# Kernel optimization log

Hardware: AMD Instinct MI355X
Metric: run time of the kernel (lower is better)

Reference implementation:

```python
import jax, jax.numpy as jnp
import numpy as np

R = 8          # shuffle_rate
HEADS = 4
DIM_HEAD = 64


def setup_inputs() -> dict:
    key = jax.random.key(0)
    k1, k2, k3 = jax.random.split(key, 3)
    dim = 64
    C = dim * R * R            # 4096, token channel dim after unshuffle
    inner = HEADS * DIM_HEAD   # 256
    x = jax.random.normal(k1, (8, dim, 256, 256), dtype=jnp.float32)
    W_qkv = jax.random.normal(k2, (C, 3 * inner), dtype=jnp.float32) * (C ** -0.5)
    W_out = jax.random.normal(k3, (inner, C), dtype=jnp.float32) * (inner ** -0.5)
    b_out = jnp.zeros((C,), dtype=jnp.float32)
    return {"x": x, "W_qkv": W_qkv, "W_out": W_out, "b_out": b_out}


def reference(x, W_qkv, W_out, b_out):
    scale = DIM_HEAD ** -0.5
    B, C0, H0, W0 = x.shape
    h, w = H0 // R, W0 // R
    N = h * w
    C = C0 * R * R
    # PixelUnshuffle: [B,C0,H0,W0] -> [B, C0*R*R, h, w]
    xd = x.reshape(B, C0, h, R, w, R).transpose(0, 1, 3, 5, 2, 4).reshape(B, C, h, w)
    # flatten spatial -> tokens [B, N, C]
    tokens = xd.reshape(B, C, N).transpose(0, 2, 1)
    qkv = tokens @ W_qkv                                   # [B, N, 3*inner]
    q, k, v = jnp.split(qkv, 3, axis=-1)
    def heads(t):  # [B,N,inner] -> [B,H,N,d]
        return t.reshape(B, N, HEADS, DIM_HEAD).transpose(0, 2, 1, 3)
    q, k, v = heads(q), heads(k), heads(v)
    dots = jnp.einsum('bhnd,bhmd->bhnm', q, k) * scale
    attn = jax.nn.softmax(dots, axis=-1)
    out = jnp.einsum('bhnm,bhmd->bhnd', attn, v)
    out = out.transpose(0, 2, 1, 3).reshape(B, N, HEADS * DIM_HEAD)
    y = out @ W_out + b_out                                # [B, N, C]
    y = y.transpose(0, 2, 1).reshape(B, C, h, w)
    # PixelShuffle: [B, C0*R*R, h, w] -> [B, C0, H0, W0]
    y = y.reshape(B, C0, R, R, h, w).transpose(0, 1, 4, 2, 5, 3).reshape(B, C0, H0, W0)
    return y
```

## Files before the change

### kernel.cpp

```cpp
#include <hip/hip_runtime.h>

typedef unsigned short u16;
typedef __attribute__((ext_vector_type(8))) short s16x8;
typedef __attribute__((ext_vector_type(4))) short s16x4;
typedef __attribute__((ext_vector_type(4))) float f32x4;

__device__ __forceinline__ u16 f2bf(float f) {
    unsigned int u;
    __builtin_memcpy(&u, &f, 4);
    unsigned int r = u + 0x7FFFu + ((u >> 16) & 1u);
    return (u16)(r >> 16);
}

__device__ __forceinline__ void gl_lds16(const u16* g, u16* l) {
    __builtin_amdgcn_global_load_lds(
        (const __attribute__((address_space(1))) unsigned int*)g,
        (__attribute__((address_space(3))) unsigned int*)l,
        16, 0, 0);
}

__global__ __launch_bounds__(256) void k_unshuffle(const float* __restrict__ x,
                                                   u16* __restrict__ tok) {
    int idx = blockIdx.x * 256 + threadIdx.x;
    int r1  = idx & 7;
    int xxg = (idx >> 3) & 7;
    int yy  = (idx >> 6) & 31;
    int c0  = (idx >> 11) & 63;
    int b   = idx >> 17;

    const float* src = x + ((size_t)((b * 64 + c0) * 256 + yy * 8 + r1)) * 256 + xxg * 32;
    int mbase = b * 1024 + yy * 32 + xxg * 4;
    int cbase = c0 * 64 + r1 * 8;
    for (int q = 0; q < 4; ++q) {
        float4 f0 = *(const float4*)(src + q * 8);
        float4 f1 = *(const float4*)(src + q * 8 + 4);
        s16x8 v;
        v[0] = (short)f2bf(f0.x); v[1] = (short)f2bf(f0.y);
        v[2] = (short)f2bf(f0.z); v[3] = (short)f2bf(f0.w);
        v[4] = (short)f2bf(f1.x); v[5] = (short)f2bf(f1.y);
        v[6] = (short)f2bf(f1.z); v[7] = (short)f2bf(f1.w);
        *(s16x8*)(tok + (size_t)(mbase + q) * 4096 + cbase) = v;
    }
}

__global__ __launch_bounds__(256) void k_transpose(const float* __restrict__ in,
                                                   u16* __restrict__ out,
                                                   int rows, int cols) {
    __shared__ float tile[64][65];
    int bx = blockIdx.x * 64, by = blockIdx.y * 64;
    int tx = threadIdx.x & 63, ty = threadIdx.x >> 6;
    for (int i = ty; i < 64; i += 4)
        tile[i][tx] = in[(size_t)(by + i) * cols + bx + tx];
    __syncthreads();
    for (int i = ty; i < 64; i += 4)
        out[(size_t)(bx + i) * rows + by + tx] = f2bf(tile[tx][i]);
}

__global__ __launch_bounds__(256) void k_gemm_qkv(const u16* __restrict__ A,
                                                  const u16* __restrict__ Bt,
                                                  float* __restrict__ P) {
    const int K = 4096;
    __shared__ u16 As[128 * 64];
    __shared__ u16 Bs[128 * 64];
    const int tid = threadIdx.x;
    const int wave = tid >> 6, lane = tid & 63;
    const int quad = lane >> 4, l15 = lane & 15;
    const int wm = wave >> 1, wn = wave & 1;
    const int tm = blockIdx.y * 128, tn = blockIdx.x * 128;
    const int z = blockIdx.z;

    f32x4 acc[4][4] = {};

    for (int k0 = z * 2048; k0 < (z + 1) * 2048; k0 += 64) {
        __syncthreads();
        for (int t = 0; t < 4; ++t) {
            int c = wave * 256 + t * 64 + lane;
            int row = c >> 3, kc = c & 7;
            gl_lds16(A + (size_t)(tm + row) * K + k0 + kc * 8,
                     As + (wave * 256 + t * 64) * 8);
        }
        for (int t = 0; t < 4; ++t) {
            int c = wave * 256 + t * 64 + lane;
            int row = c >> 3, kc = c & 7;
            gl_lds16(Bt + (size_t)(tn + row) * K + k0 + kc * 8,
                     Bs + (wave * 256 + t * 64) * 8);
        }
        __syncthreads();
        for (int kk = 0; kk < 64; kk += 32) {
            s16x8 af[4], bf[4];
            for (int i = 0; i < 4; ++i)
                af[i] = *(const s16x8*)(As + (wm * 64 + i * 16 + l15) * 64 + kk + quad * 8);
            for (int j = 0; j < 4; ++j)
                bf[j] = *(const s16x8*)(Bs + (wn * 64 + j * 16 + l15) * 64 + kk + quad * 8);
            for (int i = 0; i < 4; ++i)
                for (int j = 0; j < 4; ++j)
                    acc[i][j] = __builtin_amdgcn_mfma_f32_16x16x32_bf16(af[i], bf[j], acc[i][j], 0, 0, 0);
        }
    }

    float* Pz = P + (size_t)z * 8192 * 768;
    for (int i = 0; i < 4; ++i) {
        int mb = tm + wm * 64 + i * 16 + quad * 4;
        for (int j = 0; j < 4; ++j) {
            int col = tn + wn * 64 + j * 16 + l15;
            for (int r = 0; r < 4; ++r)
                Pz[(size_t)(mb + r) * 768 + col] = acc[i][j][r];
        }
    }
}

__global__ __launch_bounds__(256) void k_qkv_reduce(const float* __restrict__ P,
                                                    u16* __restrict__ Qo,
                                                    u16* __restrict__ Ko,
                                                    u16* __restrict__ Vt) {
    __shared__ u16 tile[64][65];
    const int tid = threadIdx.x;
    const int ct = blockIdx.x, mt = blockIdx.y;
    const int c_l = tid & 63;
    const int col = ct * 64 + c_l;
    const int mbase = mt * 64;
    const float* P1 = P + (size_t)8192 * 768;

    if (ct < 8) {
        int which = col >> 8;
        int h = (col >> 6) & 3, d = col & 63;
        u16* dst = (which == 0) ? Qo : Ko;
        for (int k = 0; k < 16; ++k) {
            int m = mbase + (tid >> 6) + k * 4;
            float v = P[(size_t)m * 768 + col] + P1[(size_t)m * 768 + col];
            int b = m >> 10, n = m & 1023;
            dst[((size_t)((b * 4 + h) * 1024 + n)) * 64 + d] = f2bf(v);
        }
    } else {
        int h = ct - 8;
        int b = mbase >> 10;
        int nbase = mbase & 1023;
        for (int k = 0; k < 16; ++k) {
            int ml = (tid >> 6) + k * 4;
            int m = mbase + ml;
            float v = P[(size_t)m * 768 + col] + P1[(size_t)m * 768 + col];
            tile[ml][c_l] = f2bf(v);
        }
        __syncthreads();
        for (int k = 0; k < 16; ++k) {
            int d = (tid >> 6) + k * 4;
            Vt[((size_t)((b * 4 + h) * 64 + d)) * 1024 + nbase + c_l] = tile[c_l][d];
        }
    }
}

__global__ __launch_bounds__(256) void k_attn(const u16* __restrict__ Qb,
                                              const u16* __restrict__ Kb,
                                              const u16* __restrict__ Vt,
                                              u16* __restrict__ aout) {
    const int bh = blockIdx.y;
    const int q0 = blockIdx.x * 64;
    const int tid = threadIdx.x;
    const int wave = tid >> 6, lane = tid & 63;
    const int quad = lane >> 4, l15 = lane & 15;
    const size_t base = (size_t)bh * 1024 * 64;
    const float scale = 0.125f;

    __shared__ u16 Ks[64 * 64];
    __shared__ u16 Vts[64 * 68];
    __shared__ u16 Ps[4][16 * 64];

    s16x8 aq0, aq1;
    {
        const u16* qp = Qb + base + (size_t)(q0 + wave * 16 + l15) * 64 + quad * 8;
        aq0 = *(const s16x8*)(qp);
        aq1 = *(const s16x8*)(qp + 32);
    }

    float m_i[4], l_i[4];
    f32x4 o[4] = {};
    for (int r = 0; r < 4; ++r) { m_i[r] = -1e30f; l_i[r] = 0.f; }

    const int vrow = tid >> 2, vpart = tid & 3;

    for (int t = 0; t < 16; ++t) {
        __syncthreads();
        for (int e = 0; e < 2; ++e) {
            int s = e * 256 + tid;
            gl_lds16(Kb + base + (size_t)t * 4096 + s * 8, Ks + s * 8);
        }
        {
            const u16* src = Vt + base + (size_t)vrow * 1024 + t * 64 + vpart * 16;
            s16x8 a = *(const s16x8*)(src);
            s16x8 b2 = *(const s16x8*)(src + 8);
            *(s16x8*)(Vts + vrow * 68 + vpart * 16) = a;
            *(s16x8*)(Vts + vrow * 68 + vpart * 16 + 8) = b2;
        }
        __syncthreads();

        f32x4 s4[4];
        for (int j = 0; j < 4; ++j) {
            const u16* kr = Ks + (j * 16 + l15) * 64 + quad * 8;
            s16x8 b0 = *(const s16x8*)(kr);
            s16x8 b1 = *(const s16x8*)(kr + 32);
            f32x4 c = {};
            c = __builtin_amdgcn_mfma_f32_16x16x32_bf16(aq0, b0, c, 0, 0, 0);
            c = __builtin_amdgcn_mfma_f32_16x16x32_bf16(aq1, b1, c, 0, 0, 0);
            s4[j] = c;
        }

        for (int r = 0; r < 4; ++r) {
            float sv0 = s4[0][r] * scale, sv1 = s4[1][r] * scale;
            float sv2 = s4[2][r] * scale, sv3 = s4[3][r] * scale;
            float mt = fmaxf(fmaxf(sv0, sv1), fmaxf(sv2, sv3));
            for (int off = 1; off < 16; off <<= 1)
                mt = fmaxf(mt, __shfl_xor(mt, off, 64));
            float mn = fmaxf(m_i[r], mt);
            float alpha = __expf(m_i[r] - mn);
            m_i[r] = mn;
            float p0 = __expf(sv0 - mn), p1 = __expf(sv1 - mn);
            float p2 = __expf(sv2 - mn), p3 = __expf(sv3 - mn);
            u16* pw = Ps[wave] + (quad * 4 + r) * 64 + l15;
            pw[0]  = f2bf(p0);
            pw[16] = f2bf(p1);
            pw[32] = f2bf(p2);
            pw[48] = f2bf(p3);
            float rs = p0 + p1 + p2 + p3;
            for (int off = 1; off < 16; off <<= 1)
                rs += __shfl_xor(rs, off, 64);
            l_i[r] = l_i[r] * alpha + rs;
            for (int dt = 0; dt < 4; ++dt) o[dt][r] *= alpha;
        }

        for (int kk = 0; kk < 64; kk += 32) {
            s16x8 pf = *(const s16x8*)(Ps[wave] + l15 * 64 + kk + quad * 8);
            for (int dt = 0; dt < 4; ++dt) {
                const u16* vr = Vts + (dt * 16 + l15) * 68 + kk + quad * 8;
                s16x4 v0 = *(const s16x4*)(vr);
                s16x4 v1 = *(const s16x4*)(vr + 4);
                s16x8 vf;
                vf[0] = v0[0]; vf[1] = v0[1]; vf[2] = v0[2]; vf[3] = v0[3];
                vf[4] = v1[0]; vf[5] = v1[1]; vf[6] = v1[2]; vf[7] = v1[3];
                o[dt] = __builtin_amdgcn_mfma_f32_16x16x32_bf16(pf, vf, o[dt], 0, 0, 0);
            }
        }
    }

    int b = bh >> 2, h = bh & 3;
    float rl[4];
    for (int r = 0; r < 4; ++r) rl[r] = 1.0f / l_i[r];
    for (int dt = 0; dt < 4; ++dt)
        for (int r = 0; r < 4; ++r) {
            int qrow = q0 + wave * 16 + quad * 4 + r;
            aout[((size_t)(b) * 1024 + qrow) * 256 + h * 64 + dt * 16 + l15] =
                f2bf(o[dt][r] * rl[r]);
        }
}

__global__ __launch_bounds__(256) void k_gemm_out(const u16* __restrict__ A,
                                                  const u16* __restrict__ Bt,
                                                  const float* __restrict__ bias,
                                                  float* __restrict__ out) {
    const int K = 256;
    __shared__ u16 As[128 * 64];
    __shared__ u16 Bs[128 * 64];
    const int tid = threadIdx.x;
    const int wave = tid >> 6, lane = tid & 63;
    const int quad = lane >> 4, l15 = lane & 15;
    const int wm = wave >> 1, wn = wave & 1;
    const int tm = blockIdx.y * 128, tn = blockIdx.x * 128;

    f32x4 acc[4][4] = {};

    for (int k0 = 0; k0 < K; k0 += 64) {
        __syncthreads();
        for (int t = 0; t < 4; ++t) {
            int c = wave * 256 + t * 64 + lane;
            int row = c >> 3, kc = c & 7;
            gl_lds16(A + (size_t)(tm + row) * K + k0 + kc * 8,
                     As + (wave * 256 + t * 64) * 8);
        }
        for (int t = 0; t < 4; ++t) {
            int c = wave * 256 + t * 64 + lane;
            int row = c >> 3, kc = c & 7;
            gl_lds16(Bt + (size_t)(tn + row) * K + k0 + kc * 8,
                     Bs + (wave * 256 + t * 64) * 8);
        }
        __syncthreads();
        for (int kk = 0; kk < 64; kk += 32) {
            s16x8 af[4], bf[4];
            for (int i = 0; i < 4; ++i)
                af[i] = *(const s16x8*)(As + (wm * 64 + i * 16 + l15) * 64 + kk + quad * 8);
            for (int j = 0; j < 4; ++j)
                bf[j] = *(const s16x8*)(Bs + (wn * 64 + j * 16 + l15) * 64 + kk + quad * 8);
            for (int i = 0; i < 4; ++i)
                for (int j = 0; j < 4; ++j)
                    acc[i][j] = __builtin_amdgcn_mfma_f32_16x16x32_bf16(af[i], bf[j], acc[i][j], 0, 0, 0);
        }
    }

    for (int i = 0; i < 4; ++i) {
        int mb = tm + wm * 64 + i * 16 + quad * 4;
        for (int j = 0; j < 4; ++j) {
            int col = tn + wn * 64 + j * 16 + l15;
            float bb = bias[col];
            int c0 = col >> 6, r1 = (col >> 3) & 7, r2 = col & 7;
            for (int r = 0; r < 4; ++r) {
                int m = mb + r;
                int b = m >> 10, n = m & 1023, yy = n >> 5, xx = n & 31;
                size_t oidx = ((size_t)((b * 64 + c0) * 256 + yy * 8 + r1)) * 256 + xx * 8 + r2;
                out[oidx] = acc[i][j][r] + bb;
            }
        }
    }
}

extern "C" void kernel_launch(void* const* d_in, const int* in_sizes, int n_in,
                              void* d_out, int out_size, void* d_ws, size_t ws_size,
                              hipStream_t stream) {
    (void)in_sizes; (void)n_in; (void)out_size; (void)ws_size;
    const float* x    = (const float*)d_in[0];
    const float* Wqkv = (const float*)d_in[1];
    const float* Wout = (const float*)d_in[2];
    const float* bout = (const float*)d_in[3];
    float* out = (float*)d_out;

    u16* ws     = (u16*)d_ws;
    u16* tokens = ws;
    u16* wqkvT  = tokens + 33554432;
    u16* woutT  = wqkvT + 3145728;
    u16* Qb     = woutT + 1048576;
    u16* Kb     = Qb + 2097152;
    u16* Vtb    = Kb + 2097152;
    u16* aoutb  = Vtb + 2097152;
    float* Pp   = (float*)(aoutb + 2097152);

    k_unshuffle<<<4096, 256, 0, stream>>>(x, tokens);
    k_transpose<<<dim3(12, 64), 256, 0, stream>>>(Wqkv, wqkvT, 4096, 768);
    k_transpose<<<dim3(64, 4), 256, 0, stream>>>(Wout, woutT, 256, 4096);
    k_gemm_qkv<<<dim3(6, 64, 2), 256, 0, stream>>>(tokens, wqkvT, Pp);
    k_qkv_reduce<<<dim3(12, 128), 256, 0, stream>>>(Pp, Qb, Kb, Vtb);
    k_attn<<<dim3(16, 32), 256, 0, stream>>>(Qb, Kb, Vtb, aoutb);
    k_gemm_out<<<dim3(32, 64), 256, 0, stream>>>(aoutb, woutT, bout, out);
}
```

Measured before the change: 419.5 us.

## Fuse pixel-unshuffle and bf16 conversion into the QKV GEMM A-tile load

```diff
diff --git a/kernel.cpp b/kernel.cpp
--- a/kernel.cpp
+++ b/kernel.cpp
@@ -12,35 +12,17 @@
     return (u16)(r >> 16);
 }
 
+__device__ __forceinline__ unsigned int cvt_pk_bf16(float a, float b) {
+    unsigned int r;
+    asm("v_cvt_pk_bf16_f32 %0, %1, %2" : "=v"(r) : "v"(a), "v"(b));
+    return r;
+}
+
 __device__ __forceinline__ void gl_lds16(const u16* g, u16* l) {
     __builtin_amdgcn_global_load_lds(
         (const __attribute__((address_space(1))) unsigned int*)g,
         (__attribute__((address_space(3))) unsigned int*)l,
         16, 0, 0);
-}
-
-__global__ __launch_bounds__(256) void k_unshuffle(const float* __restrict__ x,
-                                                   u16* __restrict__ tok) {
-    int idx = blockIdx.x * 256 + threadIdx.x;
-    int r1  = idx & 7;
-    int xxg = (idx >> 3) & 7;
-    int yy  = (idx >> 6) & 31;
-    int c0  = (idx >> 11) & 63;
-    int b   = idx >> 17;
-
-    const float* src = x + ((size_t)((b * 64 + c0) * 256 + yy * 8 + r1)) * 256 + xxg * 32;
-    int mbase = b * 1024 + yy * 32 + xxg * 4;
-    int cbase = c0 * 64 + r1 * 8;
-    for (int q = 0; q < 4; ++q) {
-        float4 f0 = *(const float4*)(src + q * 8);
-        float4 f1 = *(const float4*)(src + q * 8 + 4);
-        s16x8 v;
-        v[0] = (short)f2bf(f0.x); v[1] = (short)f2bf(f0.y);
-        v[2] = (short)f2bf(f0.z); v[3] = (short)f2bf(f0.w);
-        v[4] = (short)f2bf(f1.x); v[5] = (short)f2bf(f1.y);
-        v[6] = (short)f2bf(f1.z); v[7] = (short)f2bf(f1.w);
-        *(s16x8*)(tok + (size_t)(mbase + q) * 4096 + cbase) = v;
-    }
 }
 
 __global__ __launch_bounds__(256) void k_transpose(const float* __restrict__ in,
@@ -56,7 +38,7 @@
         out[(size_t)(bx + i) * rows + by + tx] = f2bf(tile[tx][i]);
 }
 
-__global__ __launch_bounds__(256) void k_gemm_qkv(const u16* __restrict__ A,
+__global__ __launch_bounds__(256) void k_gemm_qkv(const float* __restrict__ x,
                                                   const u16* __restrict__ Bt,
                                                   float* __restrict__ P) {
     const int K = 4096;
@@ -66,24 +48,54 @@
     const int wave = tid >> 6, lane = tid & 63;
     const int quad = lane >> 4, l15 = lane & 15;
     const int wm = wave >> 1, wn = wave & 1;
-    const int tm = blockIdx.y * 128, tn = blockIdx.x * 128;
-    const int z = blockIdx.z;
+
+    int lin = blockIdx.x;
+    int rem = (lin & 7) * 96 + (lin >> 3);
+    int tn6 = rem % 6;
+    int rq  = rem / 6;
+    int z   = rq & 1;
+    int tmi = rq >> 1;
+    const int tm = tmi * 128, tn = tn6 * 128;
+
+    const float* aptr[4];
+#pragma unroll
+    for (int t = 0; t < 4; ++t) {
+        int cidx = wave * 256 + t * 64 + lane;
+        int row = cidx >> 3, kc = cidx & 7;
+        int m = tm + row;
+        int b = m >> 10, n = m & 1023, yy = n >> 5, xx = n & 31;
+        aptr[t] = x + (size_t)b * 4194304 + (size_t)z * 2097152
+                    + (yy * 8 + kc) * 256 + xx * 8;
+    }
 
     f32x4 acc[4][4] = {};
 
     for (int k0 = z * 2048; k0 < (z + 1) * 2048; k0 += 64) {
-        __syncthreads();
-        for (int t = 0; t < 4; ++t) {
-            int c = wave * 256 + t * 64 + lane;
-            int row = c >> 3, kc = c & 7;
-            gl_lds16(A + (size_t)(tm + row) * K + k0 + kc * 8,
-                     As + (wave * 256 + t * 64) * 8);
-        }
+        float4 va[4][2];
+#pragma unroll
+        for (int t = 0; t < 4; ++t) {
+            const float4* sp = (const float4*)aptr[t];
+            va[t][0] = sp[0];
+            va[t][1] = sp[1];
+            aptr[t] += 65536;
+        }
+        __syncthreads();
+#pragma unroll
         for (int t = 0; t < 4; ++t) {
             int c = wave * 256 + t * 64 + lane;
             int row = c >> 3, kc = c & 7;
             gl_lds16(Bt + (size_t)(tn + row) * K + k0 + kc * 8,
                      Bs + (wave * 256 + t * 64) * 8);
+        }
+#pragma unroll
+        for (int t = 0; t < 4; ++t) {
+            int cidx = wave * 256 + t * 64 + lane;
+            uint4 pk;
+            pk.x = cvt_pk_bf16(va[t][0].x, va[t][0].y);
+            pk.y = cvt_pk_bf16(va[t][0].z, va[t][0].w);
+            pk.z = cvt_pk_bf16(va[t][1].x, va[t][1].y);
+            pk.w = cvt_pk_bf16(va[t][1].z, va[t][1].w);
+            *(uint4*)(As + cidx * 8) = pk;
         }
         __syncthreads();
         for (int kk = 0; kk < 64; kk += 32) {
@@ -321,8 +333,7 @@
     float* out = (float*)d_out;
 
     u16* ws     = (u16*)d_ws;
-    u16* tokens = ws;
-    u16* wqkvT  = tokens + 33554432;
+    u16* wqkvT  = ws;
     u16* woutT  = wqkvT + 3145728;
     u16* Qb     = woutT + 1048576;
     u16* Kb     = Qb + 2097152;
@@ -330,10 +341,9 @@
     u16* aoutb  = Vtb + 2097152;
     float* Pp   = (float*)(aoutb + 2097152);
 
-    k_unshuffle<<<4096, 256, 0, stream>>>(x, tokens);
     k_transpose<<<dim3(12, 64), 256, 0, stream>>>(Wqkv, wqkvT, 4096, 768);
     k_transpose<<<dim3(64, 4), 256, 0, stream>>>(Wout, woutT, 256, 4096);
-    k_gemm_qkv<<<dim3(6, 64, 2), 256, 0, stream>>>(tokens, wqkvT, Pp);
+    k_gemm_qkv<<<dim3(768, 1, 1), 256, 0, stream>>>(x, wqkvT, Pp);
     k_qkv_reduce<<<dim3(12, 128), 256, 0, stream>>>(Pp, Qb, Kb, Vtb);
     k_attn<<<dim3(16, 32), 256, 0, stream>>>(Qb, Kb, Vtb, aoutb);
     k_gemm_out<<<dim3(32, 64), 256, 0, stream>>>(aoutb, woutT, bout, out);
```

After: 474.9 us. +13.2%, slower.
